# Kernel optimization log

Hardware: AMD Instinct MI355X
Metric: run time of the kernel (lower is better)

The kernel has to match this reference:

```python
import jax, jax.numpy as jnp
import numpy as np

NODE_DIM = 256
HID = 128
EDGE_DIM = 128
NUM_BINS = 22
MAX_LEN = 2056
TOTAL_FEATS = HID * 3 + NUM_BINS * 2 + 2


def get_index_embedding(indices, embed_size, max_len):
    # sinusoidal index embedding as in RiboFlow utils
    K = jnp.arange(embed_size // 2, dtype=jnp.float32)
    ang = indices[..., None].astype(jnp.float32) * jnp.pi / (max_len ** (2.0 * K / embed_size))
    return jnp.concatenate([jnp.sin(ang), jnp.cos(ang)], axis=-1)


def calc_distogram(pos, min_bin, max_bin, num_bins):
    # pos: [B, N, 3] -> one-hot distogram [B, N, N, num_bins]
    d = jnp.linalg.norm(pos[:, :, None, :] - pos[:, None, :, :], axis=-1)[..., None]
    lower = jnp.linspace(min_bin, max_bin, num_bins)
    upper = jnp.concatenate([lower[1:], jnp.array([1e8], dtype=jnp.float32)])
    return ((d > lower) & (d < upper)).astype(jnp.float32)


def cross_concat(f):
    # f: [B, N, D] -> [B, N, N, 2D] via row/col tiling
    B, N, D = f.shape
    return jnp.concatenate([
        jnp.broadcast_to(f[:, :, None, :], (B, N, N, D)),
        jnp.broadcast_to(f[:, None, :, :], (B, N, N, D)),
    ], axis=-1)


def _linear_params(key, fi, fo):
    s = 1.0 / np.sqrt(fi)
    kw, kb = jax.random.split(key)
    W = jax.random.uniform(kw, (fi, fo), jnp.float32, -s, s)
    b = jax.random.uniform(kb, (fo,), jnp.float32, -s, s)
    return W, b


def setup_inputs() -> dict:
    key = jax.random.key(0)
    ks = jax.random.split(key, 12)
    B, N = 1, 512
    inp = {
        'node_features': jax.random.normal(ks[0], (B, N, NODE_DIM), jnp.float32),
        'trans': jax.random.normal(ks[1], (B, N, 3), jnp.float32) * 10.0,
        'sc_trans': jax.random.normal(ks[2], (B, N, 3), jnp.float32) * 10.0,
        'edge_mask': jnp.ones((B, N, N), jnp.float32),
        'flow_mask': (jax.random.uniform(ks[4], (B, N)) > 0.5).astype(jnp.float32),
    }
    inp['W_n2e'], inp['b_n2e'] = _linear_params(ks[5], NODE_DIM, HID)
    inp['W_rp'], inp['b_rp'] = _linear_params(ks[6], HID, HID)
    inp['W1'], inp['b1'] = _linear_params(ks[7], TOTAL_FEATS, EDGE_DIM)
    inp['W2'], inp['b2'] = _linear_params(ks[8], EDGE_DIM, EDGE_DIM)
    inp['W3'], inp['b3'] = _linear_params(ks[9], EDGE_DIM, EDGE_DIM)
    inp['ln_g'] = jnp.ones((EDGE_DIM,), jnp.float32)
    inp['ln_b'] = jnp.zeros((EDGE_DIM,), jnp.float32)
    return inp


def reference(node_features, trans, sc_trans, edge_mask, flow_mask,
              W_n2e, b_n2e, W_rp, b_rp, W1, b1, W2, b2, W3, b3, ln_g, ln_b):
    B, N, _ = node_features.shape
    # node -> edge projection, then cross-concat tiling: [B,N,N,2*HID]
    n2e = node_features @ W_n2e + b_n2e
    pair_node_feats = cross_concat(n2e)
    # relative position sinusoidal embedding + linear: [B,N,N,HID]
    seq = jnp.arange(N, dtype=jnp.float32)
    relpos = jnp.broadcast_to(seq[None, :, None] - seq[None, None, :], (B, N, N))
    relpos_feats = get_index_embedding(relpos, HID, MAX_LEN) @ W_rp + b_rp
    # distograms: [B,N,N,NUM_BINS] each
    dist_feats = calc_distogram(trans, 0.001, 20.0, NUM_BINS)
    sc_feats = calc_distogram(sc_trans, 0.001, 20.0, NUM_BINS)
    # flow mask pair features: [B,N,N,2]
    flow_feat = cross_concat(flow_mask[..., None])
    feats = jnp.concatenate([pair_node_feats, relpos_feats, dist_feats, sc_feats, flow_feat], axis=-1)
    # 3-layer MLP + LayerNorm
    h = jax.nn.relu(feats @ W1 + b1)
    h = jax.nn.relu(h @ W2 + b2)
    h = h @ W3 + b3
    mu = jnp.mean(h, axis=-1, keepdims=True)
    var = jnp.var(h, axis=-1, keepdims=True)
    h = (h - mu) * jax.lax.rsqrt(var + 1e-5) * ln_g + ln_b
    return h * edge_mask[..., None]
```

## Files before the change

kernel.cpp:

```cpp
#include <hip/hip_runtime.h>


using bf16x8 = __attribute__((ext_vector_type(8))) short;
using f32x4  = __attribute__((ext_vector_type(4))) float;

__device__ __forceinline__ unsigned short f2bf(float f) {
    unsigned int u;
    __builtin_memcpy(&u, &f, 4);
    unsigned int r = (u + 0x7fffu + ((u >> 16) & 1u)) >> 16;
    return (unsigned short)r;
}

__global__ void pre_node(const float* __restrict__ nf,
                         const float* __restrict__ Wn2e,
                         const float* __restrict__ bn2e,
                         const float* __restrict__ W1,
                         const float* __restrict__ b1,
                         const float* __restrict__ flow,
                         float* __restrict__ A, float* __restrict__ Bv)
{
    __shared__ float nfs[256];
    __shared__ float n2s[128];
    const int i = blockIdx.x, f = threadIdx.x;
    nfs[f]       = nf[i * 256 + f];
    nfs[f + 128] = nf[i * 256 + 128 + f];
    __syncthreads();
    float acc = bn2e[f];
    for (int k = 0; k < 256; k++) acc += nfs[k] * Wn2e[k * 128 + f];
    n2s[f] = acc;
    __syncthreads();
    const float fl = flow[i];
    float aA = b1[f] + fl * W1[428 * 128 + f];
    float aB =         fl * W1[429 * 128 + f];
    for (int k = 0; k < 128; k++) {
        const float s = n2s[k];
        aA += s * W1[k * 128 + f];
        aB += s * W1[(128 + k) * 128 + f];
    }
    A[i * 128 + f]  = aA;
    Bv[i * 128 + f] = aB;
}

__global__ void pre_rel(const float* __restrict__ Wrp,
                        const float* __restrict__ brp,
                        const float* __restrict__ W1,
                        float* __restrict__ Rm)
{
    __shared__ float emb[128];
    __shared__ float rp[128];
    const int dix = blockIdx.x;
    const float d = (float)(dix - 511);
    const int m = threadIdx.x;
    const int K = m & 63;
    const float denom = powf(2056.0f, (float)K * (1.0f / 64.0f));
    const float ang = d * 3.14159265358979323846f / denom;
    emb[m] = (m < 64) ? sinf(ang) : cosf(ang);
    __syncthreads();
    float acc = brp[m];
    for (int k = 0; k < 128; k++) acc += emb[k] * Wrp[k * 128 + m];
    rp[m] = acc;
    __syncthreads();
    float acc2 = 0.0f;
    for (int k = 0; k < 128; k++) acc2 += rp[k] * W1[(256 + k) * 128 + m];
    Rm[dix * 128 + m] = acc2;
}

__global__ __launch_bounds__(512, 2) void edge_main(
    const float* __restrict__ trans,
    const float* __restrict__ sctrans,
    const float* __restrict__ emask,
    const float* __restrict__ W1,
    const float* __restrict__ W2,
    const float* __restrict__ b2,
    const float* __restrict__ W3,
    const float* __restrict__ b3,
    const float* __restrict__ lng,
    const float* __restrict__ lnb,
    const float* __restrict__ A,
    const float* __restrict__ Bv,
    const float* __restrict__ Rm,
    float* __restrict__ out)
{
    __shared__ __align__(16) short W2L[16 * 128 * 8];
    __shared__ __align__(16) short W3L[16 * 128 * 8];
    __shared__ __align__(16) short hbuf[256 * 136];
    __shared__ __align__(16) float As[128];
    __shared__ int binsD[256];
    __shared__ int binsS[256];

    const int tid = threadIdx.x;
    const int i  = blockIdx.x >> 1;
    const int j0 = (blockIdx.x & 1) << 8;

    for (int idx = tid; idx < 16384; idx += 512) {
        const int k = idx >> 7, n = idx & 127;
        const int dst = ((k >> 3) * 128 + n) * 8 + (k & 7);
        W2L[dst] = (short)f2bf(W2[idx]);
        W3L[dst] = (short)f2bf(W3[idx]);
    }
    if (tid < 128) As[tid] = A[i * 128 + tid];

    {
        const int p = tid & 255;
        const float* P = (tid < 256) ? trans : sctrans;
        const int j = j0 + p;
        const float dx = __fsub_rn(P[i * 3 + 0], P[j * 3 + 0]);
        const float dy = __fsub_rn(P[i * 3 + 1], P[j * 3 + 1]);
        const float dz = __fsub_rn(P[i * 3 + 2], P[j * 3 + 2]);
        const float d2 = __fadd_rn(__fadd_rn(__fmul_rn(dx, dx), __fmul_rn(dy, dy)),
                                   __fmul_rn(dz, dz));
        const double dd = (double)sqrtf(d2);
        const double step = (20.0 - 0.001) / 21.0;
        int bin = -1;
        for (int b = 0; b < 22; b++) {
            const double lo = (b == 21) ? 20.0 : __dadd_rn(0.001, __dmul_rn((double)b, step));
            const double up = (b == 20) ? 20.0 :
                              ((b == 21) ? 1e8 : __dadd_rn(0.001, __dmul_rn((double)(b + 1), step)));
            if (dd > lo && dd < up) bin = b;
        }
        if (tid < 256) binsD[p] = bin; else binsS[p] = bin;
    }
    __syncthreads();

    const int w = tid >> 6;
    const int l = tid & 63;
    const int q = l >> 4;
    const int ln16 = l & 15;

    for (int it = 0; it < 16; it++) {
        const int flat = it * 64 + l;
        const int p = 32 * w + (flat >> 5);
        const int f = (flat & 31) << 2;
        const int j = j0 + p;
        const int didx = i - j + 511;
        const f32x4 bv = *(const f32x4*)&Bv[j * 128 + f];
        const f32x4 r  = *(const f32x4*)&Rm[didx * 128 + f];
        const f32x4 a  = *(const f32x4*)&As[f];
        const int bD = binsD[p], bS = binsS[p];
        const float sD = bD >= 0 ? 1.0f : 0.0f;
        const float sS = bS >= 0 ? 1.0f : 0.0f;
        const int rD = 384 + (bD >= 0 ? bD : 0);
        const int rS = 406 + (bS >= 0 ? bS : 0);
        const f32x4 wd  = *(const f32x4*)&W1[rD * 128 + f];
        const f32x4 wsv = *(const f32x4*)&W1[rS * 128 + f];
        float h0 = a.x + bv.x + r.x + sD * wd.x + sS * wsv.x;
        float h1 = a.y + bv.y + r.y + sD * wd.y + sS * wsv.y;
        float h2 = a.z + bv.z + r.z + sD * wd.z + sS * wsv.z;
        float h3 = a.w + bv.w + r.w + sD * wd.w + sS * wsv.w;
        h0 = fmaxf(h0, 0.0f); h1 = fmaxf(h1, 0.0f);
        h2 = fmaxf(h2, 0.0f); h3 = fmaxf(h3, 0.0f);
        uint2 pk;
        pk.x = (unsigned int)f2bf(h0) | ((unsigned int)f2bf(h1) << 16);
        pk.y = (unsigned int)f2bf(h2) | ((unsigned int)f2bf(h3) << 16);
        *(uint2*)&hbuf[p * 136 + f] = pk;
    }
    __syncthreads();

    bf16x8 af[2][4];
    for (int mt = 0; mt < 2; mt++)
        for (int kb = 0; kb < 4; kb++)
            af[mt][kb] = *(const bf16x8*)&hbuf[(32 * w + mt * 16 + ln16) * 136 + q * 8 + kb * 32];

    const f32x4 vzero = {0.0f, 0.0f, 0.0f, 0.0f};
    f32x4 acc[2][8];
    for (int mt = 0; mt < 2; mt++)
        for (int nb = 0; nb < 8; nb++) acc[mt][nb] = vzero;

    for (int nb = 0; nb < 8; nb++) {
        for (int kb = 0; kb < 4; kb++) {
            const bf16x8 bfrg = *(const bf16x8*)&W2L[((kb * 4 + q) * 128 + nb * 16 + ln16) * 8];
            acc[0][nb] = __builtin_amdgcn_mfma_f32_16x16x32_bf16(af[0][kb], bfrg, acc[0][nb], 0, 0, 0);
            acc[1][nb] = __builtin_amdgcn_mfma_f32_16x16x32_bf16(af[1][kb], bfrg, acc[1][nb], 0, 0, 0);
        }
    }
    __syncthreads();

    float b2v[8];
    for (int nb = 0; nb < 8; nb++) b2v[nb] = b2[nb * 16 + ln16];
    for (int nb = 0; nb < 8; nb++)
        for (int mt = 0; mt < 2; mt++)
            for (int rg = 0; rg < 4; rg++) {
                float v = acc[mt][nb][rg] + b2v[nb];
                v = fmaxf(v, 0.0f);
                const int p = 32 * w + mt * 16 + q * 4 + rg;
                hbuf[p * 136 + nb * 16 + ln16] = (short)f2bf(v);
            }
    __syncthreads();

    for (int mt = 0; mt < 2; mt++)
        for (int kb = 0; kb < 4; kb++)
            af[mt][kb] = *(const bf16x8*)&hbuf[(32 * w + mt * 16 + ln16) * 136 + q * 8 + kb * 32];
    for (int mt = 0; mt < 2; mt++)
        for (int nb = 0; nb < 8; nb++) acc[mt][nb] = vzero;
    for (int nb = 0; nb < 8; nb++) {
        for (int kb = 0; kb < 4; kb++) {
            const bf16x8 bfrg = *(const bf16x8*)&W3L[((kb * 4 + q) * 128 + nb * 16 + ln16) * 8];
            acc[0][nb] = __builtin_amdgcn_mfma_f32_16x16x32_bf16(af[0][kb], bfrg, acc[0][nb], 0, 0, 0);
            acc[1][nb] = __builtin_amdgcn_mfma_f32_16x16x32_bf16(af[1][kb], bfrg, acc[1][nb], 0, 0, 0);
        }
    }

    float b3v[8], gv[8], bbv[8];
    for (int nb = 0; nb < 8; nb++) {
        const int n = nb * 16 + ln16;
        b3v[nb] = b3[n];
        gv[nb]  = lng[n];
        bbv[nb] = lnb[n];
    }
    for (int mt = 0; mt < 2; mt++) {
        for (int rg = 0; rg < 4; rg++) {
            float v[8];
            float s = 0.0f;
            for (int nb = 0; nb < 8; nb++) { v[nb] = acc[mt][nb][rg] + b3v[nb]; s += v[nb]; }
            for (int m = 1; m < 16; m <<= 1) s += __shfl_xor(s, m, 64);
            const float mu = s * (1.0f / 128.0f);
            float ss = 0.0f;
            for (int nb = 0; nb < 8; nb++) { const float dv = v[nb] - mu; ss += dv * dv; }
            for (int m = 1; m < 16; m <<= 1) ss += __shfl_xor(ss, m, 64);
            const float rstd = rsqrtf(ss * (1.0f / 128.0f) + 1e-5f);
            const int p = 32 * w + mt * 16 + q * 4 + rg;
            const int j = j0 + p;
            const float msk = emask[i * 512 + j];
            const int obase = (i * 512 + j) * 128;
            for (int nb = 0; nb < 8; nb++) {
                const float o = ((v[nb] - mu) * rstd * gv[nb] + bbv[nb]) * msk;
                out[obase + nb * 16 + ln16] = o;
            }
        }
    }
}

extern "C" void kernel_launch(void* const* d_in, const int* in_sizes, int n_in,
                              void* d_out, int out_size, void* d_ws, size_t ws_size,
                              hipStream_t stream)
{
    const float* nf    = (const float*)d_in[0];
    const float* trans = (const float*)d_in[1];
    const float* sctr  = (const float*)d_in[2];
    const float* emask = (const float*)d_in[3];
    const float* flow  = (const float*)d_in[4];
    const float* Wn2e  = (const float*)d_in[5];
    const float* bn2e  = (const float*)d_in[6];
    const float* Wrp   = (const float*)d_in[7];
    const float* brp   = (const float*)d_in[8];
    const float* W1    = (const float*)d_in[9];
    const float* b1    = (const float*)d_in[10];
    const float* W2    = (const float*)d_in[11];
    const float* b2    = (const float*)d_in[12];
    const float* W3    = (const float*)d_in[13];
    const float* b3    = (const float*)d_in[14];
    const float* lng   = (const float*)d_in[15];
    const float* lnb   = (const float*)d_in[16];

    float* ws = (float*)d_ws;
    float* A  = ws;
    float* Bv = ws + 512 * 128;
    float* Rm = ws + 2 * 512 * 128;
    float* out = (float*)d_out;

    pre_node<<<512, 128, 0, stream>>>(nf, Wn2e, bn2e, W1, b1, flow, A, Bv);
    pre_rel<<<1023, 128, 0, stream>>>(Wrp, brp, W1, Rm);
    edge_main<<<1024, 512, 0, stream>>>(trans, sctr, emask, W1, W2, b2, W3, b3,
                                        lng, lnb, A, Bv, Rm, out);
}
```

Before: 261.1 us.

## Merge preprocessing kernels, prestage bf16 weights globally, drop LDS weight copies and barriers

Fuses pre_node and pre_rel into a single pre_all launch that also converts W2/W3 to bf16 in the MFMA-friendly layout in workspace. edge_main then reads B fragments from global/cache instead of rebuilding them in LDS per block. This cuts LDS use and raises launch bounds to 4 blocks per CU. It also removes several __syncthreads, restructures the layer-2 and layer-3 accumulators to lower register pressure, and uses v_cvt_pk_bf16_f32 for packing. The barrier removal relies on each wave touching only its own hbuf rows, and global weight reads may add latency.

```diff
diff --git a/kernel.cpp b/kernel.cpp
--- a/kernel.cpp
+++ b/kernel.cpp
@@ -11,68 +11,85 @@
     return (unsigned short)r;
 }
 
-__global__ void pre_node(const float* __restrict__ nf,
-                         const float* __restrict__ Wn2e,
-                         const float* __restrict__ bn2e,
-                         const float* __restrict__ W1,
-                         const float* __restrict__ b1,
-                         const float* __restrict__ flow,
-                         float* __restrict__ A, float* __restrict__ Bv)
+__device__ __forceinline__ unsigned int cvt_pk_bf16(float lo, float hi) {
+    unsigned int r;
+    asm("v_cvt_pk_bf16_f32 %0, %1, %2" : "=v"(r) : "v"(lo), "v"(hi));
+    return r;
+}
+
+__global__ void pre_all(const float* __restrict__ nf,
+                        const float* __restrict__ Wn2e,
+                        const float* __restrict__ bn2e,
+                        const float* __restrict__ W1,
+                        const float* __restrict__ b1,
+                        const float* __restrict__ flow,
+                        const float* __restrict__ Wrp,
+                        const float* __restrict__ brp,
+                        const float* __restrict__ W2,
+                        const float* __restrict__ W3,
+                        float* __restrict__ A, float* __restrict__ Bv,
+                        float* __restrict__ Rm,
+                        short* __restrict__ W2b, short* __restrict__ W3b)
 {
-    __shared__ float nfs[256];
-    __shared__ float n2s[128];
-    const int i = blockIdx.x, f = threadIdx.x;
-    nfs[f]       = nf[i * 256 + f];
-    nfs[f + 128] = nf[i * 256 + 128 + f];
-    __syncthreads();
-    float acc = bn2e[f];
-    for (int k = 0; k < 256; k++) acc += nfs[k] * Wn2e[k * 128 + f];
-    n2s[f] = acc;
-    __syncthreads();
-    const float fl = flow[i];
-    float aA = b1[f] + fl * W1[428 * 128 + f];
-    float aB =         fl * W1[429 * 128 + f];
-    for (int k = 0; k < 128; k++) {
-        const float s = n2s[k];
-        aA += s * W1[k * 128 + f];
-        aB += s * W1[(128 + k) * 128 + f];
-    }
-    A[i * 128 + f]  = aA;
-    Bv[i * 128 + f] = aB;
-}
-
-__global__ void pre_rel(const float* __restrict__ Wrp,
-                        const float* __restrict__ brp,
-                        const float* __restrict__ W1,
-                        float* __restrict__ Rm)
-{
-    __shared__ float emb[128];
-    __shared__ float rp[128];
-    const int dix = blockIdx.x;
-    const float d = (float)(dix - 511);
+    __shared__ float s0[256];
+    __shared__ float s1[128];
+    const int bid = blockIdx.x;
     const int m = threadIdx.x;
-    const int K = m & 63;
-    const float denom = powf(2056.0f, (float)K * (1.0f / 64.0f));
-    const float ang = d * 3.14159265358979323846f / denom;
-    emb[m] = (m < 64) ? sinf(ang) : cosf(ang);
-    __syncthreads();
-    float acc = brp[m];
-    for (int k = 0; k < 128; k++) acc += emb[k] * Wrp[k * 128 + m];
-    rp[m] = acc;
-    __syncthreads();
-    float acc2 = 0.0f;
-    for (int k = 0; k < 128; k++) acc2 += rp[k] * W1[(256 + k) * 128 + m];
-    Rm[dix * 128 + m] = acc2;
-}
-
-__global__ __launch_bounds__(512, 2) void edge_main(
+
+    if (bid < 512) {
+        const int i = bid;
+        s0[m]       = nf[i * 256 + m];
+        s0[m + 128] = nf[i * 256 + 128 + m];
+        __syncthreads();
+        float acc = bn2e[m];
+        for (int k = 0; k < 256; k++) acc += s0[k] * Wn2e[k * 128 + m];
+        s1[m] = acc;
+        __syncthreads();
+        const float fl = flow[i];
+        float aA = b1[m] + fl * W1[428 * 128 + m];
+        float aB =         fl * W1[429 * 128 + m];
+        for (int k = 0; k < 128; k++) {
+            const float s = s1[k];
+            aA += s * W1[k * 128 + m];
+            aB += s * W1[(128 + k) * 128 + m];
+        }
+        A[i * 128 + m]  = aA;
+        Bv[i * 128 + m] = aB;
+    } else if (bid < 1535) {
+        const int dix = bid - 512;
+        const float d = (float)(dix - 511);
+        const int K = m & 63;
+        const float denom = powf(2056.0f, (float)K * (1.0f / 64.0f));
+        const float ang = d * 3.14159265358979323846f / denom;
+        s0[m] = (m < 64) ? sinf(ang) : cosf(ang);
+        __syncthreads();
+        float acc = brp[m];
+        for (int k = 0; k < 128; k++) acc += s0[k] * Wrp[k * 128 + m];
+        s1[m] = acc;
+        __syncthreads();
+        float acc2 = 0.0f;
+        for (int k = 0; k < 128; k++) acc2 += s1[k] * W1[(256 + k) * 128 + m];
+        Rm[dix * 128 + m] = acc2;
+    } else {
+        const int t = (bid - 1535) * 128 + m;
+        for (int h = 0; h < 2; h++) {
+            const int idx = t + h * 8192;
+            const int k = idx >> 7, n = idx & 127;
+            const int dst = ((k >> 3) * 128 + n) * 8 + (k & 7);
+            W2b[dst] = (short)f2bf(W2[idx]);
+            W3b[dst] = (short)f2bf(W3[idx]);
+        }
+    }
+}
+
+__global__ __launch_bounds__(512, 4) void edge_main(
     const float* __restrict__ trans,
     const float* __restrict__ sctrans,
     const float* __restrict__ emask,
     const float* __restrict__ W1,
-    const float* __restrict__ W2,
+    const short* __restrict__ W2b,
     const float* __restrict__ b2,
-    const float* __restrict__ W3,
+    const short* __restrict__ W3b,
     const float* __restrict__ b3,
     const float* __restrict__ lng,
     const float* __restrict__ lnb,
@@ -81,8 +98,6 @@
     const float* __restrict__ Rm,
     float* __restrict__ out)
 {
-    __shared__ __align__(16) short W2L[16 * 128 * 8];
-    __shared__ __align__(16) short W3L[16 * 128 * 8];
     __shared__ __align__(16) short hbuf[256 * 136];
     __shared__ __align__(16) float As[128];
     __shared__ int binsD[256];
@@ -92,12 +107,6 @@
     const int i  = blockIdx.x >> 1;
     const int j0 = (blockIdx.x & 1) << 8;
 
-    for (int idx = tid; idx < 16384; idx += 512) {
-        const int k = idx >> 7, n = idx & 127;
-        const int dst = ((k >> 3) * 128 + n) * 8 + (k & 7);
-        W2L[dst] = (short)f2bf(W2[idx]);
-        W3L[dst] = (short)f2bf(W3[idx]);
-    }
     if (tid < 128) As[tid] = A[i * 128 + tid];
 
     {
@@ -150,11 +159,10 @@
         h0 = fmaxf(h0, 0.0f); h1 = fmaxf(h1, 0.0f);
         h2 = fmaxf(h2, 0.0f); h3 = fmaxf(h3, 0.0f);
         uint2 pk;
-        pk.x = (unsigned int)f2bf(h0) | ((unsigned int)f2bf(h1) << 16);
-        pk.y = (unsigned int)f2bf(h2) | ((unsigned int)f2bf(h3) << 16);
+        pk.x = cvt_pk_bf16(h0, h1);
+        pk.y = cvt_pk_bf16(h2, h3);
         *(uint2*)&hbuf[p * 136 + f] = pk;
     }
-    __syncthreads();
 
     bf16x8 af[2][4];
     for (int mt = 0; mt < 2; mt++)
@@ -162,61 +170,52 @@
             af[mt][kb] = *(const bf16x8*)&hbuf[(32 * w + mt * 16 + ln16) * 136 + q * 8 + kb * 32];
 
     const f32x4 vzero = {0.0f, 0.0f, 0.0f, 0.0f};
-    f32x4 acc[2][8];
-    for (int mt = 0; mt < 2; mt++)
-        for (int nb = 0; nb < 8; nb++) acc[mt][nb] = vzero;
 
     for (int nb = 0; nb < 8; nb++) {
+        f32x4 a0 = vzero, a1 = vzero;
         for (int kb = 0; kb < 4; kb++) {
-            const bf16x8 bfrg = *(const bf16x8*)&W2L[((kb * 4 + q) * 128 + nb * 16 + ln16) * 8];
-            acc[0][nb] = __builtin_amdgcn_mfma_f32_16x16x32_bf16(af[0][kb], bfrg, acc[0][nb], 0, 0, 0);
-            acc[1][nb] = __builtin_amdgcn_mfma_f32_16x16x32_bf16(af[1][kb], bfrg, acc[1][nb], 0, 0, 0);
-        }
-    }
-    __syncthreads();
-
-    float b2v[8];
-    for (int nb = 0; nb < 8; nb++) b2v[nb] = b2[nb * 16 + ln16];
-    for (int nb = 0; nb < 8; nb++)
-        for (int mt = 0; mt < 2; mt++)
-            for (int rg = 0; rg < 4; rg++) {
-                float v = acc[mt][nb][rg] + b2v[nb];
-                v = fmaxf(v, 0.0f);
-                const int p = 32 * w + mt * 16 + q * 4 + rg;
-                hbuf[p * 136 + nb * 16 + ln16] = (short)f2bf(v);
+            const bf16x8 bfrg = *(const bf16x8*)&W2b[((kb * 4 + q) * 128 + nb * 16 + ln16) * 8];
+            a0 = __builtin_amdgcn_mfma_f32_16x16x32_bf16(af[0][kb], bfrg, a0, 0, 0, 0);
+            a1 = __builtin_amdgcn_mfma_f32_16x16x32_bf16(af[1][kb], bfrg, a1, 0, 0, 0);
+        }
+        const float b2v = b2[nb * 16 + ln16];
+        for (int rg = 0; rg < 4; rg++) {
+            const float v0 = fmaxf(a0[rg] + b2v, 0.0f);
+            const float v1 = fmaxf(a1[rg] + b2v, 0.0f);
+            hbuf[(32 * w +      q * 4 + rg) * 136 + nb * 16 + ln16] = (short)cvt_pk_bf16(v0, v0);
+            hbuf[(32 * w + 16 + q * 4 + rg) * 136 + nb * 16 + ln16] = (short)cvt_pk_bf16(v1, v1);
+        }
+    }
+
+    for (int mt = 0; mt < 2; mt++) {
+        bf16x8 a3[4];
+        for (int kb = 0; kb < 4; kb++)
+            a3[kb] = *(const bf16x8*)&hbuf[(32 * w + mt * 16 + ln16) * 136 + q * 8 + kb * 32];
+
+        f32x4 acc3[8];
+        for (int nb = 0; nb < 8; nb++) acc3[nb] = vzero;
+        for (int nb = 0; nb < 8; nb++)
+            for (int kb = 0; kb < 4; kb++) {
+                const bf16x8 bfrg = *(const bf16x8*)&W3b[((kb * 4 + q) * 128 + nb * 16 + ln16) * 8];
+                acc3[nb] = __builtin_amdgcn_mfma_f32_16x16x32_bf16(a3[kb], bfrg, acc3[nb], 0, 0, 0);
             }
-    __syncthreads();
-
-    for (int mt = 0; mt < 2; mt++)
-        for (int kb = 0; kb < 4; kb++)
-            af[mt][kb] = *(const bf16x8*)&hbuf[(32 * w + mt * 16 + ln16) * 136 + q * 8 + kb * 32];
-    for (int mt = 0; mt < 2; mt++)
-        for (int nb = 0; nb < 8; nb++) acc[mt][nb] = vzero;
-    for (int nb = 0; nb < 8; nb++) {
-        for (int kb = 0; kb < 4; kb++) {
-            const bf16x8 bfrg = *(const bf16x8*)&W3L[((kb * 4 + q) * 128 + nb * 16 + ln16) * 8];
-            acc[0][nb] = __builtin_amdgcn_mfma_f32_16x16x32_bf16(af[0][kb], bfrg, acc[0][nb], 0, 0, 0);
-            acc[1][nb] = __builtin_amdgcn_mfma_f32_16x16x32_bf16(af[1][kb], bfrg, acc[1][nb], 0, 0, 0);
-        }
-    }
-
-    float b3v[8], gv[8], bbv[8];
-    for (int nb = 0; nb < 8; nb++) {
-        const int n = nb * 16 + ln16;
-        b3v[nb] = b3[n];
-        gv[nb]  = lng[n];
-        bbv[nb] = lnb[n];
-    }
-    for (int mt = 0; mt < 2; mt++) {
+
+        float b3v[8], gv[8], bbv[8];
+        for (int nb = 0; nb < 8; nb++) {
+            const int n = nb * 16 + ln16;
+            b3v[nb] = b3[n];
+            gv[nb]  = lng[n];
+            bbv[nb] = lnb[n];
+        }
         for (int rg = 0; rg < 4; rg++) {
             float v[8];
             float s = 0.0f;
-            for (int nb = 0; nb < 8; nb++) { v[nb] = acc[mt][nb][rg] + b3v[nb]; s += v[nb]; }
-            for (int m = 1; m < 16; m <<= 1) s += __shfl_xor(s, m, 64);
+            for (int nb = 0; nb < 8; nb++) { v[nb] = acc3[nb][rg] + b3v[nb]; s += v[nb]; }
+            for (int mm = 1; mm < 16; mm <<= 1) s += __shfl_xor(s, mm, 64);
             const float mu = s * (1.0f / 128.0f);
             float ss = 0.0f;
             for (int nb = 0; nb < 8; nb++) { const float dv = v[nb] - mu; ss += dv * dv; }
-            for (int m = 1; m < 16; m <<= 1) ss += __shfl_xor(ss, m, 64);
+            for (int mm = 1; mm < 16; mm <<= 1) ss += __shfl_xor(ss, mm, 64);
             const float rstd = rsqrtf(ss * (1.0f / 128.0f) + 1e-5f);
             const int p = 32 * w + mt * 16 + q * 4 + rg;
             const int j = j0 + p;
@@ -253,13 +252,15 @@
     const float* lnb   = (const float*)d_in[16];
 
     float* ws = (float*)d_ws;
-    float* A  = ws;
-    float* Bv = ws + 512 * 128;
-    float* Rm = ws + 2 * 512 * 128;
+    float* A   = ws;
+    float* Bv  = ws + 512 * 128;
+    float* Rm  = ws + 2 * 512 * 128;
+    short* W2b = (short*)(ws + 262016);
+    short* W3b = (short*)(ws + 270208);
     float* out = (float*)d_out;
 
-    pre_node<<<512, 128, 0, stream>>>(nf, Wn2e, bn2e, W1, b1, flow, A, Bv);
-    pre_rel<<<1023, 128, 0, stream>>>(Wrp, brp, W1, Rm);
-    edge_main<<<1024, 512, 0, stream>>>(trans, sctr, emask, W1, W2, b2, W3, b3,
+    pre_all<<<1599, 128, 0, stream>>>(nf, Wn2e, bn2e, W1, b1, flow, Wrp, brp,
+                                      W2, W3, A, Bv, Rm, W2b, W3b);
+    edge_main<<<1024, 512, 0, stream>>>(trans, sctr, emask, W1, W2b, b2, W3b, b3,
                                         lng, lnb, A, Bv, Rm, out);
 }
```

Result: no change. 265.6 us (+1.7%).
